# Kernel tuning notes

Measured on AMD Instinct MI355X. Metric: run time of the kernel, lower is better.

## Reference

```python
import jax, jax.numpy as jnp
import numpy as np

H = 64  # LSTM hidden size


def _conv1d_same(x, w, b):
    # x: [B, C_in, L], w: [C_out, C_in, K], 'same' padding, stride 1
    y = jax.lax.conv_general_dilated(
        x, w, window_strides=(1,), padding='SAME',
        dimension_numbers=('NCW', 'OIW', 'NCW'))
    return y + b[None, :, None]


def _maxpool2(x):
    # x: [B, C, L] -> kernel 2, stride 2, floor
    B, C, L = x.shape
    L2 = (L // 2) * 2
    return x[:, :, :L2].reshape(B, C, L2 // 2, 2).max(axis=-1)


def _lstm_layer(x, w_ih, w_hh, b_ih, b_hh):
    # x: [B, T, I]; PyTorch gate order i, f, g, o stacked along first dim (4H)
    B, T, _ = x.shape
    xp = jnp.einsum('bti,gi->btg', x, w_ih) + (b_ih + b_hh)  # [B, T, 4H]

    def step(carry, xt):
        h, c = carry
        g = xt + h @ w_hh.T
        i, f, gg, o = jnp.split(g, 4, axis=-1)
        i = jax.nn.sigmoid(i)
        f = jax.nn.sigmoid(f)
        gg = jnp.tanh(gg)
        o = jax.nn.sigmoid(o)
        c_new = f * c + i * gg
        h_new = o * jnp.tanh(c_new)
        return (h_new, c_new), h_new

    h0 = jnp.zeros((B, H), x.dtype)
    (_, _), hs = jax.lax.scan(step, (h0, h0), jnp.swapaxes(xp, 0, 1))
    return jnp.swapaxes(hs, 0, 1)  # [B, T, H]


def setup_inputs() -> dict:
    key = jax.random.key(0)
    ks = jax.random.split(key, 16)
    s = 0.1
    d = {
        'x': jax.random.normal(ks[0], (256, 2048, 3), jnp.float32),
        'conv1_w': jax.random.normal(ks[1], (16, 3, 3), jnp.float32) * s,
        'conv1_b': jax.random.normal(ks[2], (16,), jnp.float32) * s,
        'conv2_w': jax.random.normal(ks[3], (32, 16, 3), jnp.float32) * s,
        'conv2_b': jax.random.normal(ks[4], (32,), jnp.float32) * s,
        'w_ih0': jax.random.normal(ks[5], (4 * H, 32), jnp.float32) * s,
        'w_hh0': jax.random.normal(ks[6], (4 * H, H), jnp.float32) * s,
        'b_ih0': jax.random.normal(ks[7], (4 * H,), jnp.float32) * s,
        'b_hh0': jax.random.normal(ks[8], (4 * H,), jnp.float32) * s,
        'w_ih1': jax.random.normal(ks[9], (4 * H, H), jnp.float32) * s,
        'w_hh1': jax.random.normal(ks[10], (4 * H, H), jnp.float32) * s,
        'b_ih1': jax.random.normal(ks[11], (4 * H,), jnp.float32) * s,
        'b_hh1': jax.random.normal(ks[12], (4 * H,), jnp.float32) * s,
        'fc_w': jax.random.normal(ks[13], (5, H), jnp.float32) * s,
        'fc_b': jax.random.normal(ks[14], (5,), jnp.float32) * s,
    }
    return d


def reference(x, conv1_w, conv1_b, conv2_w, conv2_b,
              w_ih0, w_hh0, b_ih0, b_hh0,
              w_ih1, w_hh1, b_ih1, b_hh1,
              fc_w, fc_b):
    h = jnp.swapaxes(x, 1, 2)             # [B, 3, T]
    h = _conv1d_same(h, conv1_w, conv1_b)  # [B, 16, T]
    h = _maxpool2(h)                       # [B, 16, T/2]
    h = _conv1d_same(h, conv2_w, conv2_b)  # [B, 32, T/2]
    h = _maxpool2(h)                       # [B, 32, T/4]
    h = jnp.swapaxes(h, 1, 2)              # [B, T/4, 32]
    h = _lstm_layer(h, w_ih0, w_hh0, b_ih0, b_hh0)
    h = _lstm_layer(h, w_ih1, w_hh1, b_ih1, b_hh1)
    return h[:, -1] @ fc_w.T + fc_b        # [B, 5]
```

## Files before the change

kernel.cpp:

```cpp
#include <hip/hip_runtime.h>

#define TSTEPS 512
#define HID    64

typedef _Float16 f16x2 __attribute__((ext_vector_type(2)));

#if __has_builtin(__builtin_amdgcn_exp2f)
#define EXP2F(x) __builtin_amdgcn_exp2f(x)
#else
#define EXP2F(x) exp2f(x)
#endif
#if __has_builtin(__builtin_amdgcn_rcpf)
#define RCPF(x) __builtin_amdgcn_rcpf(x)
#else
#define RCPF(x) (1.0f / (x))
#endif

#define CL   1.4426950408889634f
#define C2L  2.8853900817779268f
#define C4L  5.7707801635558536f

#define DPP_ADD(x, ctrl)                                                       \
  x += __int_as_float(                                                         \
      __builtin_amdgcn_mov_dpp(__float_as_int(x), (ctrl), 0xf, 0xf, true))

#if __has_builtin(__builtin_amdgcn_fdot2)
#define FDOT2(acc, a, b) acc = __builtin_amdgcn_fdot2((a), (b), (acc), false)
#else
#define FDOT2(acc, a, b)                                                       \
  acc = fmaf((float)(a).x, (float)(b).x,                                       \
             fmaf((float)(a).y, (float)(b).y, (acc)))
#endif

__device__ __forceinline__ f16x2 pk2(float a, float b, float sc) {
  return (f16x2){(_Float16)(a * sc), (_Float16)(b * sc)};
}

__device__ __forceinline__ void ldh4(const void* p, f16x2& a, f16x2& b,
                                     f16x2& c, f16x2& d) {
  const uint4 t = *(const uint4*)p;
  a = __builtin_bit_cast(f16x2, t.x);
  b = __builtin_bit_cast(f16x2, t.y);
  c = __builtin_bit_cast(f16x2, t.z);
  d = __builtin_bit_cast(f16x2, t.w);
}

__global__ __launch_bounds__(512, 1) void fused_all(
    const float* __restrict__ x,
    const float* __restrict__ c1w, const float* __restrict__ c1b,
    const float* __restrict__ c2w, const float* __restrict__ c2b,
    const float* __restrict__ w_ih0, const float* __restrict__ w_hh0,
    const float* __restrict__ b_ih0, const float* __restrict__ b_hh0,
    const float* __restrict__ w_ih1, const float* __restrict__ w_hh1,
    const float* __restrict__ b_ih1, const float* __restrict__ b_hh1,
    const float* __restrict__ fc_w, const float* __restrict__ fc_b,
    float* __restrict__ t1g, float* __restrict__ out) {
  __shared__ __align__(16) _Float16 featB[512 * 32];
  __shared__ float ws1[144];
  __shared__ float bs1[16];
  __shared__ float ws2[1536];
  __shared__ float bs2[32];
  __shared__ __align__(16) _Float16 h0s[2][64];
  __shared__ __align__(16) _Float16 h1s[2][64];

  const int tid = threadIdx.x;
  const int b = blockIdx.x;

  if (tid < 144) ws1[tid] = c1w[tid];
  if (tid < 16)  bs1[tid] = c1b[tid];
  for (int i = tid; i < 1536; i += 512) ws2[i] = c2w[i];
  if (tid < 32)  bs2[tid] = c2b[tid];
  __syncthreads();

  const float* xb = x + (size_t)b * 2048 * 3;
  float* t1b = t1g + (size_t)b * 1024 * 16;
#pragma unroll
  for (int rep = 0; rep < 2; ++rep) {
    const int t2 = rep * 512 + tid;
    const int p0 = 2 * t2;
    float xv[4][3];
#pragma unroll
    for (int j = 0; j < 4; ++j) {
      const int p = p0 - 1 + j;
      const bool ok = (p >= 0) && (p < 2048);
#pragma unroll
      for (int c = 0; c < 3; ++c) xv[j][c] = ok ? xb[p * 3 + c] : 0.0f;
    }
    float4 o4[4];
    float* op = (float*)o4;
#pragma unroll
    for (int o = 0; o < 16; ++o) {
      float s0 = bs1[o], s1 = bs1[o];
#pragma unroll
      for (int c = 0; c < 3; ++c) {
#pragma unroll
        for (int k = 0; k < 3; ++k) {
          const float wv = ws1[(o * 3 + c) * 3 + k];
          s0 = fmaf(xv[k][c],     wv, s0);
          s1 = fmaf(xv[k + 1][c], wv, s1);
        }
      }
      op[o] = fmaxf(s0, s1);
    }
    float4* dst = (float4*)(t1b + (size_t)t2 * 16);
    dst[0] = o4[0]; dst[1] = o4[1]; dst[2] = o4[2]; dst[3] = o4[3];
  }
  __syncthreads();

  {
    const int t2 = tid;
    const int p0 = 2 * t2;
    float4 r4[4][4];
    float* r = (float*)r4;
#pragma unroll
    for (int j = 0; j < 4; ++j) {
      const int p = p0 - 1 + j;
      if (p >= 0 && p < 1024) {
        const float4* s = (const float4*)(t1b + p * 16);
        r4[j][0] = s[0]; r4[j][1] = s[1]; r4[j][2] = s[2]; r4[j][3] = s[3];
      } else {
        const float4 z = {0.f, 0.f, 0.f, 0.f};
        r4[j][0] = z; r4[j][1] = z; r4[j][2] = z; r4[j][3] = z;
      }
    }
    _Float16* dst = featB + (size_t)t2 * 32;
#pragma unroll 4
    for (int o = 0; o < 32; ++o) {
      float s0 = bs2[o], s1 = bs2[o];
      const float* wo = &ws2[o * 48];
#pragma unroll
      for (int c = 0; c < 16; ++c) {
        const float w0 = wo[c * 3], w1 = wo[c * 3 + 1], w2 = wo[c * 3 + 2];
        s0 = fmaf(r[0 * 16 + c], w0, s0);
        s0 = fmaf(r[1 * 16 + c], w1, s0);
        s0 = fmaf(r[2 * 16 + c], w2, s0);
        s1 = fmaf(r[1 * 16 + c], w0, s1);
        s1 = fmaf(r[2 * 16 + c], w1, s1);
        s1 = fmaf(r[3 * 16 + c], w2, s1);
      }
      dst[o] = (_Float16)fmaxf(s0, s1);
    }
  }

  const int layer = tid >> 8;
  const int lt  = tid & 255;
  const int u = lt >> 2;
  const int q = lt & 3;

  f16x2 wx[32], wh[32];
  float bi[4];
  if (layer == 0) {
#pragma unroll
    for (int j = 0; j < 4; ++j) {
      const int rrow = j * 64 + u;
      const float sc = (j == 2) ? C2L : CL;
      const float4* px = (const float4*)(w_ih0 + (size_t)rrow * 32 + q * 8);
      const float4 p0 = px[0], p1 = px[1];
      wx[j * 4 + 0] = pk2(p0.x, p0.y, sc);
      wx[j * 4 + 1] = pk2(p0.z, p0.w, sc);
      wx[j * 4 + 2] = pk2(p1.x, p1.y, sc);
      wx[j * 4 + 3] = pk2(p1.z, p1.w, sc);
      const float4* ph = (const float4*)(w_hh0 + (size_t)rrow * 64 + q * 16);
#pragma unroll
      for (int k = 0; k < 4; ++k) {
        const float4 tw = ph[k];
        wh[j * 8 + 2 * k]     = pk2(tw.x, tw.y, sc);
        wh[j * 8 + 2 * k + 1] = pk2(tw.z, tw.w, sc);
      }
      const float bsc = (b_ih0[rrow] + b_hh0[rrow]) * sc;
      bi[j] = (q == 0) ? bsc : 0.0f;
    }
  } else {
#pragma unroll
    for (int j = 0; j < 4; ++j) {
      const int rrow = j * 64 + u;
      const float sc = (j == 2) ? C2L : CL;
      const float4* px = (const float4*)(w_ih1 + (size_t)rrow * 64 + q * 16);
#pragma unroll
      for (int k = 0; k < 4; ++k) {
        const float4 tw = px[k];
        wx[j * 8 + 2 * k]     = pk2(tw.x, tw.y, sc);
        wx[j * 8 + 2 * k + 1] = pk2(tw.z, tw.w, sc);
      }
      const float4* ph = (const float4*)(w_hh1 + (size_t)rrow * 64 + q * 16);
#pragma unroll
      for (int k = 0; k < 4; ++k) {
        const float4 tw = ph[k];
        wh[j * 8 + 2 * k]     = pk2(tw.x, tw.y, sc);
        wh[j * 8 + 2 * k + 1] = pk2(tw.z, tw.w, sc);
      }
      const float bsc = (b_ih1[rrow] + b_hh1[rrow]) * sc;
      bi[j] = (q == 0) ? bsc : 0.0f;
    }
  }

  if (tid < 64) {
    h0s[0][tid] = (_Float16)0.f; h0s[1][tid] = (_Float16)0.f;
    h1s[0][tid] = (_Float16)0.f; h1s[1][tid] = (_Float16)0.f;
  }

  __syncthreads();

  float cc = 0.0f;

  for (int t = 0; t <= TSTEPS; ++t) {
    f16x2 xa0, xa1, xa2, xa3;
    if (layer == 0 && t < TSTEPS) {
      ldh4(featB + t * 32 + q * 8, xa0, xa1, xa2, xa3);
    }
    __syncthreads();

    const bool active = layer ? (t >= 1) : (t < TSTEPS);
    if (active) {
      float a0 = bi[0], a1 = bi[1], a2 = bi[2], a3 = bi[3];
      if (layer == 0) {
        const _Float16* hp = h0s[(t + 1) & 1] + q * 16;
        f16x2 hv[8];
        ldh4(hp,     hv[0], hv[1], hv[2], hv[3]);
        ldh4(hp + 8, hv[4], hv[5], hv[6], hv[7]);
        FDOT2(a0, wx[0],  xa0); FDOT2(a0, wx[1],  xa1);
        FDOT2(a0, wx[2],  xa2); FDOT2(a0, wx[3],  xa3);
        FDOT2(a1, wx[4],  xa0); FDOT2(a1, wx[5],  xa1);
        FDOT2(a1, wx[6],  xa2); FDOT2(a1, wx[7],  xa3);
        FDOT2(a2, wx[8],  xa0); FDOT2(a2, wx[9],  xa1);
        FDOT2(a2, wx[10], xa2); FDOT2(a2, wx[11], xa3);
        FDOT2(a3, wx[12], xa0); FDOT2(a3, wx[13], xa1);
        FDOT2(a3, wx[14], xa2); FDOT2(a3, wx[15], xa3);
#pragma unroll
        for (int dd = 0; dd < 8; ++dd) {
          FDOT2(a0, wh[dd],      hv[dd]);
          FDOT2(a1, wh[8 + dd],  hv[dd]);
          FDOT2(a2, wh[16 + dd], hv[dd]);
          FDOT2(a3, wh[24 + dd], hv[dd]);
        }
      } else {
        const _Float16* xp = h0s[(t + 1) & 1] + q * 16;
        f16x2 xv[8];
        ldh4(xp,     xv[0], xv[1], xv[2], xv[3]);
        ldh4(xp + 8, xv[4], xv[5], xv[6], xv[7]);
        const _Float16* hp = h1s[t & 1] + q * 16;
        f16x2 hv[8];
        ldh4(hp,     hv[0], hv[1], hv[2], hv[3]);
        ldh4(hp + 8, hv[4], hv[5], hv[6], hv[7]);
#pragma unroll
        for (int dd = 0; dd < 8; ++dd) {
          FDOT2(a0, wx[dd],      xv[dd]);
          FDOT2(a1, wx[8 + dd],  xv[dd]);
          FDOT2(a2, wx[16 + dd], xv[dd]);
          FDOT2(a3, wx[24 + dd], xv[dd]);
        }
#pragma unroll
        for (int dd = 0; dd < 8; ++dd) {
          FDOT2(a0, wh[dd],      hv[dd]);
          FDOT2(a1, wh[8 + dd],  hv[dd]);
          FDOT2(a2, wh[16 + dd], hv[dd]);
          FDOT2(a3, wh[24 + dd], hv[dd]);
        }
      }

      DPP_ADD(a0, 0xB1); DPP_ADD(a1, 0xB1); DPP_ADD(a2, 0xB1); DPP_ADD(a3, 0xB1);
      DPP_ADD(a0, 0x4E); DPP_ADD(a1, 0x4E); DPP_ADD(a2, 0x4E); DPP_ADD(a3, 0x4E);

      const float ii = RCPF(1.0f + EXP2F(-a0));
      const float ff = RCPF(1.0f + EXP2F(-a1));
      const float gs = fmaf(-C4L, RCPF(1.0f + EXP2F(a2)), C2L);
      const float oo = RCPF(1.0f + EXP2F(-a3));
      cc = fmaf(ff, cc, ii * gs);
      const float th = fmaf(-2.0f, RCPF(1.0f + EXP2F(cc)), 1.0f);
      const float hnew = oo * th;
      if (q == 0) {
        if (layer == 0) h0s[t & 1][u] = (_Float16)hnew;
        else            h1s[(t + 1) & 1][u] = (_Float16)hnew;
      }
    }
  }
  __syncthreads();

  if (tid < 5) {
    const _Float16* h = h1s[(TSTEPS + 1) & 1];
    float s = fc_b[tid];
    const float* wrow = fc_w + tid * HID;
#pragma unroll
    for (int j = 0; j < HID; ++j) s = fmaf(wrow[j], (float)h[j], s);
    out[b * 5 + tid] = s;
  }
}

extern "C" void kernel_launch(void* const* d_in, const int* in_sizes, int n_in,
                              void* d_out, int out_size, void* d_ws, size_t ws_size,
                              hipStream_t stream) {
  (void)in_sizes; (void)n_in; (void)out_size; (void)ws_size;
  const float* x    = (const float*)d_in[0];
  const float* c1w  = (const float*)d_in[1];
  const float* c1b  = (const float*)d_in[2];
  const float* c2w  = (const float*)d_in[3];
  const float* c2b  = (const float*)d_in[4];
  const float* wih0 = (const float*)d_in[5];
  const float* whh0 = (const float*)d_in[6];
  const float* bih0 = (const float*)d_in[7];
  const float* bhh0 = (const float*)d_in[8];
  const float* wih1 = (const float*)d_in[9];
  const float* whh1 = (const float*)d_in[10];
  const float* bih1 = (const float*)d_in[11];
  const float* bhh1 = (const float*)d_in[12];
  const float* fcw  = (const float*)d_in[13];
  const float* fcb  = (const float*)d_in[14];
  float* out = (float*)d_out;

  float* t1 = (float*)d_ws;

  fused_all<<<256, 512, 0, stream>>>(x, c1w, c1b, c2w, c2b,
                                     wih0, whh0, bih0, bhh0,
                                     wih1, whh1, bih1, bhh1,
                                     fcw, fcb, t1, out);
}
```

Before: 376.5 us.

## Replace per-step block barriers with per-wave LDS counters and ring buffers

```diff
diff --git a/kernel.cpp b/kernel.cpp
--- a/kernel.cpp
+++ b/kernel.cpp
@@ -43,6 +43,19 @@
   b = __builtin_bit_cast(f16x2, t.y);
   c = __builtin_bit_cast(f16x2, t.z);
   d = __builtin_bit_cast(f16x2, t.w);
+}
+
+__device__ __forceinline__ void wait_ge(volatile unsigned int* c, int need) {
+  if (need <= 0) return;
+  for (int spin = 0; spin < 4096; ++spin) {
+    const unsigned m0 = c[0], m1 = c[1], m2 = c[2], m3 = c[3];
+    unsigned m = m0 < m1 ? m0 : m1;
+    const unsigned n = m2 < m3 ? m2 : m3;
+    m = m < n ? m : n;
+    if ((int)m >= need) break;
+  }
+  asm volatile("" ::: "memory");
+  __builtin_amdgcn_sched_barrier(0);
 }
 
 __global__ __launch_bounds__(512, 1) void fused_all(
@@ -60,8 +73,10 @@
   __shared__ float bs1[16];
   __shared__ float ws2[1536];
   __shared__ float bs2[32];
-  __shared__ __align__(16) _Float16 h0s[2][64];
-  __shared__ __align__(16) _Float16 h1s[2][64];
+  __shared__ __align__(16) _Float16 h0r[4][64];
+  __shared__ __align__(16) _Float16 h1r[4][64];
+  __shared__ __align__(16) unsigned int c0s[4];
+  __shared__ __align__(16) unsigned int c1s[4];
 
   const int tid = threadIdx.x;
   const int b = blockIdx.x;
@@ -70,6 +85,11 @@
   if (tid < 16)  bs1[tid] = c1b[tid];
   for (int i = tid; i < 1536; i += 512) ws2[i] = c2w[i];
   if (tid < 32)  bs2[tid] = c2b[tid];
+  if (tid < 4) { c0s[tid] = 0; c1s[tid] = 0; }
+  if (tid < 256) {
+    ((_Float16*)h0r)[tid] = (_Float16)0.f;
+    ((_Float16*)h1r)[tid] = (_Float16)0.f;
+  }
   __syncthreads();
 
   const float* xb = x + (size_t)b * 2048 * 3;
@@ -143,6 +163,7 @@
   }
 
   const int layer = tid >> 8;
+  const int wv = tid >> 6;
   const int lt  = tid & 255;
   const int u = lt >> 2;
   const int q = lt & 3;
@@ -194,30 +215,16 @@
     }
   }
 
-  if (tid < 64) {
-    h0s[0][tid] = (_Float16)0.f; h0s[1][tid] = (_Float16)0.f;
-    h1s[0][tid] = (_Float16)0.f; h1s[1][tid] = (_Float16)0.f;
-  }
-
   __syncthreads();
 
   float cc = 0.0f;
 
   for (int t = 0; t <= TSTEPS; ++t) {
-    f16x2 xa0, xa1, xa2, xa3;
-    if (layer == 0 && t < TSTEPS) {
-      ldh4(featB + t * 32 + q * 8, xa0, xa1, xa2, xa3);
-    }
-    __syncthreads();
-
-    const bool active = layer ? (t >= 1) : (t < TSTEPS);
-    if (active) {
-      float a0 = bi[0], a1 = bi[1], a2 = bi[2], a3 = bi[3];
-      if (layer == 0) {
-        const _Float16* hp = h0s[(t + 1) & 1] + q * 16;
-        f16x2 hv[8];
-        ldh4(hp,     hv[0], hv[1], hv[2], hv[3]);
-        ldh4(hp + 8, hv[4], hv[5], hv[6], hv[7]);
+    if (layer == 0) {
+      if (t < TSTEPS) {
+        float a0 = bi[0], a1 = bi[1], a2 = bi[2], a3 = bi[3];
+        f16x2 xa0, xa1, xa2, xa3;
+        ldh4(featB + t * 32 + q * 8, xa0, xa1, xa2, xa3);
         FDOT2(a0, wx[0],  xa0); FDOT2(a0, wx[1],  xa1);
         FDOT2(a0, wx[2],  xa2); FDOT2(a0, wx[3],  xa3);
         FDOT2(a1, wx[4],  xa0); FDOT2(a1, wx[5],  xa1);
@@ -226,6 +233,12 @@
         FDOT2(a2, wx[10], xa2); FDOT2(a2, wx[11], xa3);
         FDOT2(a3, wx[12], xa0); FDOT2(a3, wx[13], xa1);
         FDOT2(a3, wx[14], xa2); FDOT2(a3, wx[15], xa3);
+        wait_ge(c0s, t);
+        wait_ge(c1s, t - 2);
+        const _Float16* hp = h0r[(t - 1) & 3] + q * 16;
+        f16x2 hv[8];
+        ldh4(hp,     hv[0], hv[1], hv[2], hv[3]);
+        ldh4(hp + 8, hv[4], hv[5], hv[6], hv[7]);
 #pragma unroll
         for (int dd = 0; dd < 8; ++dd) {
           FDOT2(a0, wh[dd],      hv[dd]);
@@ -233,12 +246,28 @@
           FDOT2(a2, wh[16 + dd], hv[dd]);
           FDOT2(a3, wh[24 + dd], hv[dd]);
         }
-      } else {
-        const _Float16* xp = h0s[(t + 1) & 1] + q * 16;
+        DPP_ADD(a0, 0xB1); DPP_ADD(a1, 0xB1); DPP_ADD(a2, 0xB1); DPP_ADD(a3, 0xB1);
+        DPP_ADD(a0, 0x4E); DPP_ADD(a1, 0x4E); DPP_ADD(a2, 0x4E); DPP_ADD(a3, 0x4E);
+        const float ii = RCPF(1.0f + EXP2F(-a0));
+        const float ff = RCPF(1.0f + EXP2F(-a1));
+        const float gs = fmaf(-C4L, RCPF(1.0f + EXP2F(a2)), C2L);
+        const float oo = RCPF(1.0f + EXP2F(-a3));
+        cc = fmaf(ff, cc, ii * gs);
+        const float th = fmaf(-2.0f, RCPF(1.0f + EXP2F(cc)), 1.0f);
+        if (q == 0) h0r[t & 3][u] = (_Float16)(oo * th);
+      }
+      asm volatile("s_waitcnt lgkmcnt(0)" ::: "memory");
+      if ((tid & 63) == 0) c0s[wv] = (unsigned)(t + 1);
+    } else {
+      if (t >= 1) {
+        wait_ge(c0s, t);
+        wait_ge(c1s, t);
+        float a0 = bi[0], a1 = bi[1], a2 = bi[2], a3 = bi[3];
+        const _Float16* xp = h0r[(t - 1) & 3] + q * 16;
         f16x2 xv[8];
         ldh4(xp,     xv[0], xv[1], xv[2], xv[3]);
         ldh4(xp + 8, xv[4], xv[5], xv[6], xv[7]);
-        const _Float16* hp = h1s[t & 1] + q * 16;
+        const _Float16* hp = h1r[(t - 2) & 3] + q * 16;
         f16x2 hv[8];
         ldh4(hp,     hv[0], hv[1], hv[2], hv[3]);
         ldh4(hp + 8, hv[4], hv[5], hv[6], hv[7]);
@@ -256,28 +285,24 @@
           FDOT2(a2, wh[16 + dd], hv[dd]);
           FDOT2(a3, wh[24 + dd], hv[dd]);
         }
-      }
-
-      DPP_ADD(a0, 0xB1); DPP_ADD(a1, 0xB1); DPP_ADD(a2, 0xB1); DPP_ADD(a3, 0xB1);
-      DPP_ADD(a0, 0x4E); DPP_ADD(a1, 0x4E); DPP_ADD(a2, 0x4E); DPP_ADD(a3, 0x4E);
-
-      const float ii = RCPF(1.0f + EXP2F(-a0));
-      const float ff = RCPF(1.0f + EXP2F(-a1));
-      const float gs = fmaf(-C4L, RCPF(1.0f + EXP2F(a2)), C2L);
-      const float oo = RCPF(1.0f + EXP2F(-a3));
-      cc = fmaf(ff, cc, ii * gs);
-      const float th = fmaf(-2.0f, RCPF(1.0f + EXP2F(cc)), 1.0f);
-      const float hnew = oo * th;
-      if (q == 0) {
-        if (layer == 0) h0s[t & 1][u] = (_Float16)hnew;
-        else            h1s[(t + 1) & 1][u] = (_Float16)hnew;
-      }
+        DPP_ADD(a0, 0xB1); DPP_ADD(a1, 0xB1); DPP_ADD(a2, 0xB1); DPP_ADD(a3, 0xB1);
+        DPP_ADD(a0, 0x4E); DPP_ADD(a1, 0x4E); DPP_ADD(a2, 0x4E); DPP_ADD(a3, 0x4E);
+        const float ii = RCPF(1.0f + EXP2F(-a0));
+        const float ff = RCPF(1.0f + EXP2F(-a1));
+        const float gs = fmaf(-C4L, RCPF(1.0f + EXP2F(a2)), C2L);
+        const float oo = RCPF(1.0f + EXP2F(-a3));
+        cc = fmaf(ff, cc, ii * gs);
+        const float th = fmaf(-2.0f, RCPF(1.0f + EXP2F(cc)), 1.0f);
+        if (q == 0) h1r[(t - 1) & 3][u] = (_Float16)(oo * th);
+      }
+      asm volatile("s_waitcnt lgkmcnt(0)" ::: "memory");
+      if ((tid & 63) == 0) c1s[wv & 3] = (unsigned)(t + 1);
     }
   }
   __syncthreads();
 
   if (tid < 5) {
-    const _Float16* h = h1s[(TSTEPS + 1) & 1];
+    const _Float16* h = h1r[(TSTEPS - 1) & 3];
     float s = fc_b[tid];
     const float* wrow = fc_w + tid * HID;
 #pragma unroll
```

New measurement: 459.9 us. 1.22x slower.
